# Optimization experiments

Measured on AMD Instinct MI355X. Metric: run time of the kernel, lower is better.

## Reference

```python
import jax, jax.numpy as jnp
import numpy as np

EMBED = 512
HEADS = 8
DIM_HEAD = 64          # embed_dim // 8
LANDMARKS = 256        # embed_dim // 2
PINV_ITERS = 6
RES_K = 33             # nystrom residual_conv_kernel default
SCALE = DIM_HEAD ** -0.5


def layer_norm(x, g, b, eps=1e-5):
    mu = x.mean(-1, keepdims=True)
    var = ((x - mu) ** 2).mean(-1, keepdims=True)
    return (x - mu) / jnp.sqrt(var + eps) * g + b


def moore_penrose_pinv(x, iters=PINV_ITERS):
    # iterative Moore-Penrose pseudo-inverse (lucidrains nystrom-attention)
    ax = jnp.abs(x)
    z = jnp.swapaxes(x, -1, -2) / (ax.sum(-1).max() * ax.sum(-2).max())
    I = jnp.eye(x.shape[-1], dtype=x.dtype)
    for _ in range(iters):
        xz = x @ z
        z = 0.25 * z @ (13. * I - xz @ (15. * I - xz @ (7. * I - xz)))
    return z


def nystrom_attention(x, w_qkv, w_out, b_out, res_k):
    b, n, _ = x.shape
    m = LANDMARKS
    pad = (m - n % m) % m
    xp = jnp.pad(x, ((0, 0), (pad, 0), (0, 0)))  # left-pad like F.pad(..., padding, 0)
    np_ = n + pad
    qkv = (xp @ w_qkv).reshape(b, np_, 3, HEADS, DIM_HEAD)
    q = qkv[:, :, 0].transpose(0, 2, 1, 3) * SCALE   # [b,h,np,dh]
    k = qkv[:, :, 1].transpose(0, 2, 1, 3)
    v = qkv[:, :, 2].transpose(0, 2, 1, 3)
    l = np_ // m
    q_l = q.reshape(b, HEADS, m, l, DIM_HEAD).mean(3)  # [b,h,m,dh]
    k_l = k.reshape(b, HEADS, m, l, DIM_HEAD).mean(3)
    attn1 = jax.nn.softmax(jnp.einsum('bhid,bhjd->bhij', q, k_l), -1)    # [b,h,np,m]
    attn2 = jax.nn.softmax(jnp.einsum('bhid,bhjd->bhij', q_l, k_l), -1)  # [b,h,m,m]
    attn3 = jax.nn.softmax(jnp.einsum('bhid,bhjd->bhij', q_l, k), -1)    # [b,h,m,np]
    out = (attn1 @ moore_penrose_pinv(attn2)) @ (attn3 @ v)              # [b,h,np,dh]
    # depthwise residual conv over the sequence dim, per head (shared across dh)
    v_c = v.transpose(0, 3, 1, 2).reshape(b * DIM_HEAD, HEADS, np_)
    res = jax.lax.conv_general_dilated(
        v_c, res_k[:, None, :], (1,), [(RES_K // 2, RES_K // 2)],
        dimension_numbers=('NCH', 'OIH', 'NCH'), feature_group_count=HEADS)
    out = out + res.reshape(b, DIM_HEAD, HEADS, np_).transpose(0, 2, 3, 1)
    out = out.transpose(0, 2, 1, 3).reshape(b, np_, HEADS * DIM_HEAD)
    out = out @ w_out + b_out
    return out[:, -n:]  # drop left padding


def dwconv2d(x, w, b, k):
    # x: [B,C,H,W], w: [C,1,k,k] depthwise
    y = jax.lax.conv_general_dilated(
        x, w, (1, 1), [(k // 2, k // 2)] * 2,
        dimension_numbers=('NCHW', 'OIHW', 'NCHW'), feature_group_count=x.shape[1])
    return y + b[None, :, None, None]


def ppeg(x, H, W, w7, b7, w5, b5, w3, b3):
    B, _, C = x.shape
    cls_tok, feat = x[:, :1], x[:, 1:]
    f = feat.transpose(0, 2, 1).reshape(B, C, H, W)
    y = f + dwconv2d(f, w7, b7, 7) + dwconv2d(f, w5, b5, 5) + dwconv2d(f, w3, b3, 3)
    y = y.reshape(B, C, H * W).transpose(0, 2, 1)
    return jnp.concatenate([cls_tok, y], axis=1)


def reference(h, w_fc1, b_fc1, cls_token,
              ln1_g, ln1_b, qkv1_w, out1_w, out1_b, res1_k,
              conv7_w, conv7_b, conv5_w, conv5_b, conv3_w, conv3_b,
              ln2_g, ln2_b, qkv2_w, out2_w, out2_b, res2_k,
              lnf_g, lnf_b):
    h = jax.nn.relu(h @ w_fc1 + b_fc1)                 # [B,N,512]
    B, N, C = h.shape
    _H = int(np.ceil(np.sqrt(N)))
    add = _H * _H - N
    h = jnp.concatenate([h, h[:, :add]], axis=1)       # square padding
    h = jnp.concatenate([jnp.broadcast_to(cls_token, (B, 1, C)), h], axis=1)
    h = h + nystrom_attention(layer_norm(h, ln1_g, ln1_b), qkv1_w, out1_w, out1_b, res1_k)
    h = ppeg(h, _H, _H, conv7_w, conv7_b, conv5_w, conv5_b, conv3_w, conv3_b)
    h = h + nystrom_attention(layer_norm(h, ln2_g, ln2_b), qkv2_w, out2_w, out2_b, res2_k)
    return layer_norm(h, lnf_g, lnf_b)[:, 0]           # [B,512]


def setup_inputs() -> dict:
    key = jax.random.key(0)
    ks = jax.random.split(key, 24)
    B, N, IN_DIM = 2, 4096, 1024
    w = lambda k, shape, s=0.02: jax.random.normal(k, shape, jnp.float32) * s
    z = lambda shape: jnp.zeros(shape, jnp.float32)
    o = lambda shape: jnp.ones(shape, jnp.float32)
    return {
        'h': jax.random.normal(ks[0], (B, N, IN_DIM), jnp.float32),
        'w_fc1': w(ks[1], (IN_DIM, EMBED)), 'b_fc1': z((EMBED,)),
        'cls_token': w(ks[2], (1, 1, EMBED)),
        'ln1_g': o((EMBED,)), 'ln1_b': z((EMBED,)),
        'qkv1_w': w(ks[3], (EMBED, 3 * HEADS * DIM_HEAD)),
        'out1_w': w(ks[4], (HEADS * DIM_HEAD, EMBED)), 'out1_b': z((EMBED,)),
        'res1_k': w(ks[5], (HEADS, RES_K), 0.1),
        'conv7_w': w(ks[6], (EMBED, 1, 7, 7), 0.05), 'conv7_b': z((EMBED,)),
        'conv5_w': w(ks[7], (EMBED, 1, 5, 5), 0.05), 'conv5_b': z((EMBED,)),
        'conv3_w': w(ks[8], (EMBED, 1, 3, 3), 0.05), 'conv3_b': z((EMBED,)),
        'ln2_g': o((EMBED,)), 'ln2_b': z((EMBED,)),
        'qkv2_w': w(ks[9], (EMBED, 3 * HEADS * DIM_HEAD)),
        'out2_w': w(ks[10], (HEADS * DIM_HEAD, EMBED)), 'out2_b': z((EMBED,)),
        'res2_k': w(ks[11], (HEADS, RES_K), 0.1),
        'lnf_g': o((EMBED,)), 'lnf_b': z((EMBED,)),
    }
```

## Files before the change

kernel.cpp:

```cpp
#include <hip/hip_runtime.h>
#include <hip/hip_bf16.h>

#define HEADS 8
#define DH 64
#define EMB 512
#define NP 4352
#define NTOK 4097
#define PADF 255
#define LM 256
#define SCALE 0.125f

typedef __attribute__((ext_vector_type(8))) short bf8;
typedef __attribute__((ext_vector_type(4))) float f4;
typedef __attribute__((ext_vector_type(8))) unsigned short us8;
typedef __attribute__((ext_vector_type(4))) unsigned short us4;
typedef unsigned short u16;

__device__ __forceinline__ u16 f2b(float f){
  union { float f; unsigned u; } x; x.f = f;
  unsigned r = x.u + 0x7fffu + ((x.u>>16)&1u);
  return (u16)(r>>16);
}
__device__ __forceinline__ float b2f(u16 h){
  union { unsigned u; float f; } x; x.u = ((unsigned)h)<<16;
  return x.f;
}

__device__ __forceinline__ void gload_lds(const u16* g, u16* l){
  __builtin_amdgcn_global_load_lds((const __attribute__((address_space(1))) void*)g,
                                   (__attribute__((address_space(3))) void*)l, 16, 0, 0);
}

template<int MODE>
__global__ __launch_bounds__(256)
void k_g128(const u16* __restrict__ A, const u16* __restrict__ B,
            float* __restrict__ C, u16* __restrict__ C16,
            int K, int lda, int ldb, int ldc,
            long sAb, long sAh, long sBb, long sBh, long sCb, long sCh, int nh,
            float alpha, const float* __restrict__ bias, int relu, int rowoff,
            int nx, int ksplit)
{
  int z = blockIdx.z;
  const u16* Ab = A + (long)(z/nh)*sAb + (long)(z%nh)*sAh;
  const u16* Bb = B + (long)(z/nh)*sBb + (long)(z%nh)*sBh;
  long cb = (long)(z/nh)*sCb + (long)(z%nh)*sCh;
  int bx = blockIdx.x % nx, kc = blockIdx.x / nx;
  int m0 = blockIdx.y*128, n0 = bx*128;
  int klen = K/ksplit, kbeg = kc*klen, nch = klen/32;
  __shared__ u16 As[2][4096];
  __shared__ u16 Bs[2][4096];
  int tid=threadIdx.x, w=tid>>6, lane=tid&63, q=lane>>4, lr=lane&15;
  int wrow=(w>>1)*64, wcol=(w&1)*64;
  int srow = tid>>2, scol = (tid&3)*8;
  const u16* ga  = Ab + (long)(m0+srow)*lda + kbeg + scol;
  const u16* ga2 = Ab + (long)(m0+64+srow)*lda + kbeg + scol;
  const u16* gb  = Bb + (long)(n0+srow)*ldb + kbeg + scol;
  const u16* gb2 = Bb + (long)(n0+64+srow)*ldb + kbeg + scol;
  int lo = srow*32 + scol;
  f4 acc[4][4] = {};
  auto stage = [&](int r, int c){
    gload_lds(ga  + c*32, &As[r][lo]);
    gload_lds(ga2 + c*32, &As[r][2048+lo]);
    gload_lds(gb  + c*32, &Bs[r][lo]);
    gload_lds(gb2 + c*32, &Bs[r][2048+lo]);
  };
  auto compute = [&](int r){
    bf8 af[4], bfr[4];
    #pragma unroll
    for(int rr=0;rr<4;rr++) af[rr]  = *(const bf8*)&As[r][(wrow + rr*16 + lr)*32 + q*8];
    #pragma unroll
    for(int t=0;t<4;t++) bfr[t] = *(const bf8*)&Bs[r][(wcol + t*16 + lr)*32 + q*8];
    #pragma unroll
    for(int rr=0;rr<4;rr++)
      #pragma unroll
      for(int t=0;t<4;t++)
        acc[rr][t] = __builtin_amdgcn_mfma_f32_16x16x32_bf16(af[rr], bfr[t], acc[rr][t], 0,0,0);
  };
  stage(0,0);
  __syncthreads();
  for(int c=1;c<nch;c++){
    stage(c&1, c);
    compute((c-1)&1);
    __syncthreads();
  }
  compute((nch-1)&1);
  #pragma unroll
  for(int r=0;r<4;r++){
    #pragma unroll
    for(int t=0;t<4;t++){
      #pragma unroll
      for(int e=0;e<4;e++){
        int gm = m0 + wrow + r*16 + q*4 + e;
        int gn = n0 + wcol + t*16 + lr;
        float v = acc[r][t][e]*alpha;
        if(MODE==4){
          if(bias && kc==0) v += bias[gn];
          if(gm>=rowoff) atomicAdd(&C[cb + (long)(gm-rowoff)*ldc + gn], v);
        } else {
          if(bias) v += bias[gn];
          if(relu) v = fmaxf(v,0.f);
          if(MODE==0) C[cb + (long)gm*ldc + gn] = v;
          else if(MODE==2) C16[cb + (long)gm*ldc + gn] = f2b(v);
          else { if(gm>=rowoff) C[cb + (long)(gm-rowoff)*ldc + gn] += v; }
        }
      }
    }
  }
}

template<int MODE>
__global__ __launch_bounds__(256)
void k_g64(const u16* __restrict__ A, const u16* __restrict__ B,
           float* __restrict__ C, u16* __restrict__ C16,
           int K, int lda, int ldb, int ldc,
           long sAb, long sAh, long sBb, long sBh, long sCb, long sCh, int nh,
           float alpha, const float* __restrict__ bias, int rowoff, int moff,
           int nx, int ksplit)
{
  int z = blockIdx.z;
  const u16* Ab = A + (long)(z/nh)*sAb + (long)(z%nh)*sAh;
  const u16* Bb = B + (long)(z/nh)*sBb + (long)(z%nh)*sBh;
  long cb = (long)(z/nh)*sCb + (long)(z%nh)*sCh;
  int bx = blockIdx.x % nx, kc = blockIdx.x / nx;
  int m0 = blockIdx.y*64 + moff, n0 = bx*64;
  int klen = K/ksplit, kbeg = kc*klen, nch = klen/32;
  __shared__ u16 As[2][2048];
  __shared__ u16 Bs[2][2048];
  int tid=threadIdx.x, w=tid>>6, lane=tid&63, q=lane>>4, lr=lane&15;
  int srow = tid>>2, scol = (tid&3)*8;
  const u16* ga = Ab + (long)(m0+srow)*lda + kbeg + scol;
  const u16* gb = Bb + (long)(n0+srow)*ldb + kbeg + scol;
  int lo = srow*32 + scol;
  f4 acc[4] = {};
  auto stage = [&](int r, int c){
    gload_lds(ga + c*32, &As[r][lo]);
    gload_lds(gb + c*32, &Bs[r][lo]);
  };
  auto compute = [&](int r){
    bf8 af = *(const bf8*)&As[r][(w*16 + lr)*32 + q*8];
    #pragma unroll
    for(int t=0;t<4;t++){
      bf8 bfr = *(const bf8*)&Bs[r][(t*16 + lr)*32 + q*8];
      acc[t] = __builtin_amdgcn_mfma_f32_16x16x32_bf16(af, bfr, acc[t], 0,0,0);
    }
  };
  stage(0,0);
  __syncthreads();
  for(int c=1;c<nch;c++){
    stage(c&1, c);
    compute((c-1)&1);
    __syncthreads();
  }
  compute((nch-1)&1);
  #pragma unroll
  for(int t=0;t<4;t++){
    #pragma unroll
    for(int e=0;e<4;e++){
      int gm = m0 + w*16 + q*4 + e;
      int gn = n0 + t*16 + lr;
      float v = acc[t][e]*alpha;
      if(MODE==0) C[cb + (long)gm*ldc + gn] = v;
      else if(MODE==2) C16[cb + (long)gm*ldc + gn] = f2b(v);
      else if(MODE==3) atomicAdd(&C[cb + (long)gm*ldc + gn], v);
      else if(MODE==5){
        v += bias[gn];
        if(gm>=rowoff) C[cb + (long)(gm-rowoff)*ldc + gn] += v;
      }
    }
  }
}

__global__ __launch_bounds__(256)
void k_pg3(const u16* __restrict__ Ah, const u16* __restrict__ Al,
           const u16* __restrict__ Bh, const u16* __restrict__ Bl,
           u16* __restrict__ Oh, u16* __restrict__ Ol, float na, float nd,
           u16* __restrict__ TOh, u16* __restrict__ TOl, float ta, float td)
{
  long zo = (long)blockIdx.z*65536;
  int m0 = blockIdx.y*32, n0 = blockIdx.x*64;
  __shared__ u16 S[2][6144];
  int tid=threadIdx.x, w=tid>>6, lane=tid&63, q=lane>>4, lr=lane&15;
  int t2 = tid & 127;
  const u16* srcA = (tid<128 ? Ah : Al) + zo + (long)(m0 + (t2>>2))*256 + (t2&3)*8;
  const u16* srcBh = Bh + zo + (long)(n0 + (tid>>2))*256 + (tid&3)*8;
  const u16* srcBl = Bl + zo + (long)(n0 + (tid>>2))*256 + (tid&3)*8;
  f4 acc[2] = {};
  auto stage = [&](int r, int c){
    gload_lds(srcA  + c*32, &S[r][tid*8]);
    gload_lds(srcBh + c*32, &S[r][2048 + tid*8]);
    gload_lds(srcBl + c*32, &S[r][4096 + tid*8]);
  };
  int mrow = (w>>1)*16 + lr;
  auto compute = [&](int r){
    bf8 ah = *(const bf8*)&S[r][mrow*32 + q*8];
    bf8 al = *(const bf8*)&S[r][1024 + mrow*32 + q*8];
    #pragma unroll
    for(int t=0;t<2;t++){
      int nrow = (w&1)*32 + t*16 + lr;
      bf8 bh = *(const bf8*)&S[r][2048 + nrow*32 + q*8];
      bf8 bl = *(const bf8*)&S[r][4096 + nrow*32 + q*8];
      acc[t] = __builtin_amdgcn_mfma_f32_16x16x32_bf16(ah, bh, acc[t], 0,0,0);
      acc[t] = __builtin_amdgcn_mfma_f32_16x16x32_bf16(ah, bl, acc[t], 0,0,0);
      acc[t] = __builtin_amdgcn_mfma_f32_16x16x32_bf16(al, bh, acc[t], 0,0,0);
    }
  };
  stage(0,0);
  __syncthreads();
  #pragma unroll
  for(int c=1;c<8;c++){
    stage(c&1, c);
    compute((c-1)&1);
    __syncthreads();
  }
  compute(1);
  #pragma unroll
  for(int t=0;t<2;t++){
    int gn = n0 + (w&1)*32 + t*16 + lr;
    if(Oh){
      #pragma unroll
      for(int r=0;r<4;r++){
        int gm = m0 + (w>>1)*16 + q*4 + r;
        float v = na*acc[t][r] + ((gm==gn)?nd:0.f);
        u16 h = f2b(v);
        long o = zo + (long)gm*256 + gn;
        Oh[o] = h; Ol[o] = f2b(v - b2f(h));
      }
    }
    if(TOh){
      us4 th, tl;
      #pragma unroll
      for(int r=0;r<4;r++){
        int gm = m0 + (w>>1)*16 + q*4 + r;
        float v = ta*acc[t][r] + ((gm==gn)?td:0.f);
        u16 h = f2b(v);
        th[r] = h; tl[r] = f2b(v - b2f(h));
      }
      long o = zo + (long)gn*256 + (m0 + (w>>1)*16 + q*4);
      *(us4*)&TOh[o] = th; *(us4*)&TOl[o] = tl;
    }
  }
}

__global__ __launch_bounds__(256)
void k_att3(const u16* __restrict__ qkv16, const u16* __restrict__ ql,
            const u16* __restrict__ vT, float* __restrict__ partO,
            float* __restrict__ pm, float* __restrict__ pl)
{
  int kc = blockIdx.x, jt = blockIdx.y, z = blockIdx.z;
  int b = z>>3, h = z&7;
  __shared__ u16 SQ[64*64];
  __shared__ u16 SK[2][64*64];
  __shared__ u16 SV[2][64*64];
  __shared__ u16 SP[64*64];
  int tid=threadIdx.x, w=tid>>6, lane=tid&63, q=lane>>4, lr=lane&15;
  const u16* kb = qkv16 + (long)b*NP*1536 + 512 + h*64;
  const u16* vb = vT + (long)z*64*NP;
  int t00 = kc*256;
  {
    const u16* qb = ql + (long)z*16384 + jt*64*64;
    #pragma unroll
    for(int p=0;p<2;p++){
      int idx = tid + p*256; int row = idx>>3; int js = ((idx&7)^(row&7))<<3;
      gload_lds(qb + row*64 + js, &SQ[idx*8]);
    }
  }
  auto stageKV = [&](int r, int i){
    int t0 = t00 + i*64;
    #pragma unroll
    for(int p=0;p<2;p++){
      int idx = tid + p*256; int row = idx>>3; int js = ((idx&7)^(row&7))<<3;
      gload_lds(kb + (long)(t0+row)*1536 + js, &SK[r][idx*8]);
      gload_lds(vb + (long)row*NP + t0 + js, &SV[r][idx*8]);
    }
  };
  stageKV(0,0);
  __syncthreads();
  int ar = w*16+lr;
  bf8 af0 = *(const bf8*)&SQ[ar*64 + ((q^(ar&7))<<3)];
  bf8 af1 = *(const bf8*)&SQ[ar*64 + (((q|4)^(ar&7))<<3)];
  f4 o[4] = {};
  float m[4] = {-3e38f,-3e38f,-3e38f,-3e38f};
  float l[4] = {0.f,0.f,0.f,0.f};
  for(int i=0;i<4;i++){
    int cur = i&1;
    if(i<3) stageKV(cur^1, i+1);
    f4 s[4] = {};
    #pragma unroll
    for(int t=0;t<4;t++){
      int br = t*16+lr;
      bf8 b0 = *(const bf8*)&SK[cur][br*64 + ((q^(br&7))<<3)];
      bf8 b1 = *(const bf8*)&SK[cur][br*64 + (((q|4)^(br&7))<<3)];
      s[t] = __builtin_amdgcn_mfma_f32_16x16x32_bf16(af0, b0, s[t], 0,0,0);
      s[t] = __builtin_amdgcn_mfma_f32_16x16x32_bf16(af1, b1, s[t], 0,0,0);
    }
    float tm[4];
    #pragma unroll
    for(int e=0;e<4;e++) tm[e] = fmaxf(fmaxf(s[0][e],s[1][e]), fmaxf(s[2][e],s[3][e]));
    #pragma unroll
    for(int sh=1; sh<16; sh<<=1)
      #pragma unroll
      for(int e=0;e<4;e++) tm[e] = fmaxf(tm[e], __shfl_xor(tm[e], sh));
    float rs[4];
    #pragma unroll
    for(int e=0;e<4;e++){
      float mn = fmaxf(m[e], tm[e]);
      float sc = expf(m[e]-mn);
      m[e] = mn;
      l[e] *= sc;
      rs[e] = 0.f;
      o[0][e]*=sc; o[1][e]*=sc; o[2][e]*=sc; o[3][e]*=sc;
    }
    #pragma unroll
    for(int t=0;t<4;t++)
      #pragma unroll
      for(int e=0;e<4;e++){
        float p = expf(s[t][e]-m[e]);
        rs[e] += p;
        int prow = w*16+q*4+e, pcol = t*16+lr;
        SP[prow*64 + (((pcol>>3)^(prow&7))<<3) + (pcol&7)] = f2b(p);
      }
    #pragma unroll
    for(int sh=1; sh<16; sh<<=1)
      #pragma unroll
      for(int e=0;e<4;e++) rs[e] += __shfl_xor(rs[e], sh);
    #pragma unroll
    for(int e=0;e<4;e++) l[e] += rs[e];
    int pr = w*16+lr;
    #pragma unroll
    for(int ks=0;ks<2;ks++){
      bf8 pa = *(const bf8*)&SP[pr*64 + (((ks*4+q)^(pr&7))<<3)];
      #pragma unroll
      for(int t2=0;t2<4;t2++){
        int rr = t2*16+lr;
        bf8 vv = *(const bf8*)&SV[cur][rr*64 + (((ks*4+q)^(rr&7))<<3)];
        o[t2] = __builtin_amdgcn_mfma_f32_16x16x32_bf16(pa, vv, o[t2], 0,0,0);
      }
    }
    __syncthreads();
  }
  long pb = (long)(z*17+kc)*256 + jt*64 + w*16;
  #pragma unroll
  for(int e=0;e<4;e++){
    int jg = q*4+e;
    #pragma unroll
    for(int t2=0;t2<4;t2++)
      partO[(pb + jg)*64 + t2*16 + lr] = o[t2][e];
    if(lr==0){ pm[pb + jg] = m[e]; pl[pb + jg] = l[e]; }
  }
}

__global__ __launch_bounds__(128)
void k_mrg3(const float* __restrict__ partO, const float* __restrict__ pm,
            const float* __restrict__ pl, u16* __restrict__ avbT16)
{
  int jq = blockIdx.x, z = blockIdx.y, tid = threadIdx.x;
  int j0 = jq*16;
  __shared__ float wk[16][17];
  __shared__ u16 T[16][72];
  if(tid < 16){
    int j = j0 + tid;
    float mm[17];
    float M = -3e38f;
    #pragma unroll
    for(int kc=0;kc<17;kc++){ mm[kc]=pm[(z*17+kc)*256 + j]; M=fmaxf(M,mm[kc]); }
    float s = 0.f;
    #pragma unroll
    for(int kc=0;kc<17;kc++){ float e=expf(mm[kc]-M); wk[tid][kc]=e; s+=e*pl[(z*17+kc)*256 + j]; }
    float inv = 1.f/s;
    #pragma unroll
    for(int kc=0;kc<17;kc++) wk[tid][kc]*=inv;
  }
  __syncthreads();
  float acc[8];
  #pragma unroll
  for(int p=0;p<8;p++) acc[p]=0.f;
  for(int kc=0;kc<17;kc++){
    long base = ((long)(z*17+kc)*256 + j0)*64;
    #pragma unroll
    for(int p=0;p<8;p++){
      int idx = tid + p*128;
      acc[p] += wk[idx>>6][kc]*partO[base + idx];
    }
  }
  #pragma unroll
  for(int p=0;p<8;p++){ int idx = tid + p*128; T[idx>>6][idx&63] = f2b(acc[p]); }
  __syncthreads();
  int d = tid>>1, jh = (tid&1)*8;
  us8 vv;
  #pragma unroll
  for(int u=0;u<8;u++) vv[u] = T[jh+u][d];
  *(us8*)&avbT16[(long)(z*64+d)*256 + j0 + jh] = vv;
}

__global__ __launch_bounds__(256)
void k_att1(const u16* __restrict__ qkv16, const u16* __restrict__ kl,
            const u16* __restrict__ zavT, float* __restrict__ Qc)
{
  int z = blockIdx.y, b = z>>3, h = z&7;
  int m0 = blockIdx.x*64;
  __shared__ u16 SQ[64*64];
  __shared__ u16 SKL[256*64];
  __shared__ u16 SZV[64*256];
  int tid=threadIdx.x, w=tid>>6, lane=tid&63, q=lane>>4, lr=lane&15;
  {
    const u16* qb = qkv16 + (long)b*NP*1536 + h*64;
    #pragma unroll
    for(int p=0;p<2;p++){
      int idx = tid + p*256; int row = idx>>3, c8 = (idx&7)*8;
      gload_lds(qb + (long)(m0+row)*1536 + c8, &SQ[row*64 + c8]);
    }
    const u16* kb = kl + (long)z*16384;
    #pragma unroll
    for(int p=0;p<8;p++){
      int idx = tid + p*256; int row = idx>>3, c8 = (idx&7)*8;
      gload_lds(kb + row*64 + c8, &SKL[row*64 + c8]);
    }
    const u16* zb = zavT + (long)z*16384;
    #pragma unroll
    for(int p=0;p<8;p++){
      int idx = tid + p*256; int row = idx>>5, c8 = (idx&31)*8;
      gload_lds(zb + row*256 + c8, &SZV[row*256 + c8]);
    }
  }
  __syncthreads();
  f4 acc[16] = {};
  {
    bf8 af0 = *(const bf8*)&SQ[(w*16+lr)*64 + q*8];
    bf8 af1 = *(const bf8*)&SQ[(w*16+lr)*64 + 32 + q*8];
    #pragma unroll
    for(int t=0;t<16;t++){
      bf8 b0 = *(const bf8*)&SKL[(t*16+lr)*64 + q*8];
      bf8 b1 = *(const bf8*)&SKL[(t*16+lr)*64 + 32 + q*8];
      acc[t] = __builtin_amdgcn_mfma_f32_16x16x32_bf16(af0, b0, acc[t], 0,0,0);
      acc[t] = __builtin_amdgcn_mfma_f32_16x16x32_bf16(af1, b1, acc[t], 0,0,0);
    }
  }
  float mx[4] = {-1e30f,-1e30f,-1e30f,-1e30f};
  #pragma unroll
  for(int t=0;t<16;t++)
    #pragma unroll
    for(int e=0;e<4;e++) mx[e] = fmaxf(mx[e], acc[t][e]*SCALE);
  #pragma unroll
  for(int s=1;s<16;s<<=1)
    #pragma unroll
    for(int e=0;e<4;e++) mx[e] = fmaxf(mx[e], __shfl_xor(mx[e], s));
  float sm[4] = {0.f,0.f,0.f,0.f};
  #pragma unroll
  for(int t=0;t<16;t++)
    #pragma unroll
    for(int e=0;e<4;e++){ float p = expf(acc[t][e]*SCALE - mx[e]); acc[t][e]=p; sm[e]+=p; }
  #pragma unroll
  for(int s=1;s<16;s<<=1)
    #pragma unroll
    for(int e=0;e<4;e++) sm[e] += __shfl_xor(sm[e], s);
  float inv[4];
  #pragma unroll
  for(int e=0;e<4;e++) inv[e] = 1.f/sm[e];
  __syncthreads();
  u16* PS = SKL;
  #pragma unroll
  for(int t=0;t<16;t++)
    #pragma unroll
    for(int e=0;e<4;e++)
      PS[(w*16 + q*4 + e)*256 + t*16 + lr] = f2b(acc[t][e]*inv[e]);
  __syncthreads();
  f4 acc2[4] = {};
  #pragma unroll
  for(int ks=0;ks<8;ks++){
    bf8 af = *(const bf8*)&PS[(w*16+lr)*256 + ks*32 + q*8];
    #pragma unroll
    for(int t=0;t<4;t++){
      bf8 bf_ = *(const bf8*)&SZV[(t*16+lr)*256 + ks*32 + q*8];
      acc2[t] = __builtin_amdgcn_mfma_f32_16x16x32_bf16(af, bf_, acc2[t], 0,0,0);
    }
  }
  #pragma unroll
  for(int t=0;t<4;t++)
    #pragma unroll
    for(int r=0;r<4;r++){
      int gm = m0 + w*16 + q*4 + r;
      int gd = t*16 + lr;
      Qc[((long)b*NP + gm)*512 + h*64 + gd] = acc2[t][r];
    }
}

__global__ __launch_bounds__(256)
void k_smw32(float* __restrict__ X){
  long row = (long)blockIdx.x*4 + (threadIdx.x>>6);
  int lane = threadIdx.x & 63;
  float* p = X + row*256;
  float4 v = *(float4*)&p[lane*4];
  float m = fmaxf(fmaxf(v.x,v.y),fmaxf(v.z,v.w));
  for(int s=32;s;s>>=1) m = fmaxf(m, __shfl_xor(m, s));
  float e0=expf(v.x-m), e1=expf(v.y-m), e2=expf(v.z-m), e3=expf(v.w-m);
  float sum = e0+e1+e2+e3;
  for(int s=32;s;s>>=1) sum += __shfl_xor(sum, s);
  float inv = 1.f/sum;
  float4 o = {e0*inv, e1*inv, e2*inv, e3*inv};
  *(float4*)&p[lane*4] = o;
}

__global__ void k_wT(const float* __restrict__ in, u16* __restrict__ out, int K, int N){
  int n0=blockIdx.x*32, k0=blockIdx.y*32, tid=threadIdx.x;
  __shared__ float T[32][33];
  int lr=tid&31, lc=tid>>5;
  #pragma unroll
  for(int p=0;p<4;p++) T[lc+8*p][lr] = in[(long)(k0+lc+8*p)*N + n0+lr];
  __syncthreads();
  #pragma unroll
  for(int p=0;p<4;p++) out[(long)(n0+lc+8*p)*K + k0+lr] = f2b(T[lr][lc+8*p]);
}

__global__ __launch_bounds__(256)
void k_vT(const u16* __restrict__ qkv16, u16* __restrict__ vT){
  int t0=blockIdx.x*64, h=blockIdx.y, b=blockIdx.z, tid=threadIdx.x;
  __shared__ u16 T[64][72];
  const u16* src = qkv16 + (long)b*NP*1536 + 1024 + h*64;
  for(int s=0;s<2;s++){
    int idx=tid+s*256; int row=idx>>3, c8=(idx&7)*8;
    *(us8*)&T[row][c8] = *(const us8*)&src[(long)(t0+row)*1536 + c8];
  }
  __syncthreads();
  u16* dst = vT + ((long)(b*8+h)*64)*NP;
  int d = tid>>2, j0=(tid&3)*16;
  us8 v0,v1;
  #pragma unroll
  for(int jj=0;jj<8;jj++){ v0[jj]=T[j0+jj][d]; v1[jj]=T[j0+8+jj][d]; }
  *(us8*)&dst[(long)d*NP + t0 + j0]     = v0;
  *(us8*)&dst[(long)d*NP + t0 + j0 + 8] = v1;
}

__global__ void k_cvt16(const float* __restrict__ in, u16* __restrict__ out, long n){
  long i = (long)blockIdx.x*256 + threadIdx.x;
  if(i<n) out[i] = f2b(in[i]);
}

__global__ void k_cls(const float* __restrict__ cls, float* __restrict__ seq){
  int b = blockIdx.x;
  seq[(long)b*NTOK*EMB + threadIdx.x] = cls[threadIdx.x];
}

__global__ void k_ln_pad(const float* __restrict__ seq, u16* __restrict__ xp,
                         const float* __restrict__ g, const float* __restrict__ bb){
  int b = blockIdx.y, i = blockIdx.x, tid = threadIdx.x;
  u16* out = xp + ((long)b*NP + i)*EMB;
  if(i < PADF){ out[tid]=0; out[tid+256]=0; return; }
  const float* x = seq + ((long)b*NTOK + (i-PADF))*EMB;
  float v0 = x[tid], v1 = x[tid+256];
  __shared__ float red[256];
  red[tid]=v0+v1; __syncthreads();
  for(int s=128;s>0;s>>=1){ if(tid<s) red[tid]+=red[tid+s]; __syncthreads(); }
  float mu = red[0]*(1.0f/512.0f); __syncthreads();
  float d0=v0-mu, d1=v1-mu;
  red[tid]=d0*d0+d1*d1; __syncthreads();
  for(int s=128;s>0;s>>=1){ if(tid<s) red[tid]+=red[tid+s]; __syncthreads(); }
  float rstd = rsqrtf(red[0]*(1.0f/512.0f) + 1e-5f);
  out[tid]     = f2b(d0*rstd*g[tid]     + bb[tid]);
  out[tid+256] = f2b(d1*rstd*g[tid+256] + bb[tid+256]);
}

__global__ void k_landmarks(const u16* __restrict__ qkv, u16* __restrict__ q_l, u16* __restrict__ k_l){
  int j = blockIdx.x, h = blockIdx.y, b = blockIdx.z, d = threadIdx.x;
  const u16* base = qkv + (long)b*NP*1536 + h*64 + d;
  float sq=0.f, sk=0.f;
  for(int l=0;l<17;l++){
    long row = (long)(j*17+l)*1536;
    sq += b2f(base[row]);
    sk += b2f(base[row+512]);
  }
  long o = (((long)b*HEADS + h)*LM + j)*DH + d;
  q_l[o] = f2b(sq * (SCALE/17.0f));
  k_l[o] = f2b(sk * (1.0f/17.0f));
}

__global__ void k_pinv_norm(const float* __restrict__ A2, float* __restrict__ rmax, float* __restrict__ cmax){
  int z = blockIdx.x, tid = threadIdx.x;
  const float* X = A2 + (long)z*65536;
  float rs=0.f, cs=0.f;
  for(int j=0;j<256;j++){ rs += fabsf(X[tid*256+j]); cs += fabsf(X[j*256+tid]); }
  __shared__ float r1[256], r2[256];
  r1[tid]=rs; r2[tid]=cs; __syncthreads();
  for(int s=128;s>0;s>>=1){ if(tid<s){ r1[tid]=fmaxf(r1[tid],r1[tid+s]); r2[tid]=fmaxf(r2[tid],r2[tid+s]); } __syncthreads(); }
  if(tid==0){ rmax[z]=r1[0]; cmax[z]=r2[0]; }
}

__global__ void k_pair_init(const float* __restrict__ att2,
    const float* __restrict__ rmax, const float* __restrict__ cmax,
    u16* __restrict__ Xh, u16* __restrict__ Xl,
    u16* __restrict__ Zh, u16* __restrict__ Zl,
    u16* __restrict__ Zth, u16* __restrict__ Ztl)
{
  long zo = (long)blockIdx.z*65536;
  int i0 = blockIdx.y*64, j0 = blockIdx.x*64;
  float rm=0.f, cm=0.f;
  for(int t=0;t<16;t++){ rm=fmaxf(rm,rmax[t]); cm=fmaxf(cm,cmax[t]); }
  float inv = 1.0f/(rm*cm);
  __shared__ float T[64][68];
  int tid = threadIdx.x;
  int li = tid>>2, jc = (tid&3)*16;
  #pragma unroll
  for(int u=0;u<4;u++){
    float4 v = *(const float4*)&att2[zo + (long)(i0+li)*256 + j0 + jc + u*4];
    T[li][jc+u*4]=v.x; T[li][jc+u*4+1]=v.y; T[li][jc+u*4+2]=v.z; T[li][jc+u*4+3]=v.w;
    long o = zo + (long)(i0+li)*256 + j0 + jc + u*4;
    float vv[4] = {v.x,v.y,v.z,v.w};
    us4 xh, xl, zth, ztl;
    #pragma unroll
    for(int c=0;c<4;c++){
      u16 h = f2b(vv[c]); xh[c]=h; xl[c]=f2b(vv[c]-b2f(h));
      float zt = vv[c]*inv;
      u16 h2 = f2b(zt); zth[c]=h2; ztl[c]=f2b(zt-b2f(h2));
    }
    *(us4*)&Xh[o]=xh; *(us4*)&Xl[o]=xl; *(us4*)&Zth[o]=zth; *(us4*)&Ztl[o]=ztl;
  }
  __syncthreads();
  int lj = tid>>2, ic = (tid&3)*16;
  #pragma unroll
  for(int r=0;r<16;r++){
    float x = T[ic+r][lj]*inv;
    u16 h = f2b(x);
    long o = zo + (long)(j0+lj)*256 + i0 + ic + r;
    Zh[o]=h; Zl[o]=f2b(x-b2f(h));
  }
}

__global__ __launch_bounds__(256)
void k_rconv(const u16* __restrict__ qkv16, const float* __restrict__ resk,
             const float* __restrict__ Qin, u16* __restrict__ Qo16){
  int t0 = blockIdx.x*64, h = blockIdx.y, b = blockIdx.z;
  __shared__ float V[96*64];
  const u16* vb = qkv16 + (long)b*NP*1536 + 1024 + h*64;
  int tid = threadIdx.x;
  #pragma unroll
  for(int s=0;s<3;s++){
    int idx = tid + s*256;
    int row = idx>>3, c8 = (idx&7)*8;
    int p = t0 - 16 + row;
    if(p>=0 && p<NP){
      us8 v = *(const us8*)&vb[(long)p*1536 + c8];
      #pragma unroll
      for(int jj=0;jj<8;jj++) V[row*64+c8+jj] = b2f(v[jj]);
    } else {
      #pragma unroll
      for(int jj=0;jj<8;jj++) V[row*64+c8+jj] = 0.f;
    }
  }
  __syncthreads();
  int d = tid&63, lt = (tid>>6)*16;
  float acc[16] = {};
  #pragma unroll
  for(int s=0;s<48;s++){
    float val = V[(lt+s)*64 + d];
    #pragma unroll
    for(int j=0;j<16;j++){
      int tap = s - j;
      if(tap>=0 && tap<33) acc[j] += resk[h*33+tap]*val;
    }
  }
  #pragma unroll
  for(int j=0;j<16;j++){
    long idx = ((long)b*NP + t0 + lt + j)*EMB + h*64 + d;
    Qo16[idx] = f2b(Qin[idx] + acc[j]);
  }
}

__global__ __launch_bounds__(256)
void k_ppeg(const float* __restrict__ seq, float* __restrict__ out,
    const float* __restrict__ w7,const float* __restrict__ b7,
    const float* __restrict__ w5,const float* __restrict__ b5,
    const float* __restrict__ w3,const float* __restrict__ b3){
  int b = blockIdx.z, cg = blockIdx.y;
  int rp = blockIdx.x>>1, xs = blockIdx.x&1;
  int ch0 = cg*64;
  __shared__ float s7[64*49], s5[64*25], s3[64*9], sbias[64];
  int tid = threadIdx.x;
  for(int i=tid;i<64*49;i+=256) s7[i] = w7[ch0*49+i];
  for(int i=tid;i<64*25;i+=256) s5[i] = w5[ch0*25+i];
  for(int i=tid;i<64*9;i+=256)  s3[i] = w3[ch0*9+i];
  if(tid<64) sbias[tid] = b7[ch0+tid]+b5[ch0+tid]+b3[ch0+tid];
  if(cg==0 && blockIdx.x==0){
    out[(long)b*NTOK*EMB + tid]       = seq[(long)b*NTOK*EMB + tid];
    out[(long)b*NTOK*EMB + 256 + tid] = seq[(long)b*NTOK*EMB + 256 + tid];
  }
  __syncthreads();
  int c = tid & 63;
  int y = rp*4 + (tid>>6);
  const float* sbase = seq + (long)b*NTOK*EMB + EMB + (ch0 + c);
  float* obase = out + (long)b*NTOK*EMB + EMB + (ch0 + c);
  const float* W7 = &s7[c*49];
  const float* W5 = &s5[c*25];
  const float* W3 = &s3[c*9];
  float bsum = sbias[c];
  for(int xc=0;xc<4;xc++){
    int xb = xs*32 + xc*8;
    float acc[8];
    #pragma unroll
    for(int j=0;j<8;j++) acc[j] = sbase[(long)(y*64+xb+j)*EMB] + bsum;
    #pragma unroll
    for(int dy=-3;dy<=3;dy++){
      int yy = y+dy;
      if(yy<0||yy>=64) continue;
      float v[14];
      #pragma unroll
      for(int u=0;u<14;u++){
        int xx = xb + u - 3;
        v[u] = (xx>=0 && xx<64) ? sbase[(long)(yy*64+xx)*EMB] : 0.f;
      }
      #pragma unroll
      for(int dx=-3;dx<=3;dx++){
        float wsum = W7[(dy+3)*7+(dx+3)];
        if(dy>=-2&&dy<=2&&dx>=-2&&dx<=2) wsum += W5[(dy+2)*5+(dx+2)];
        if(dy>=-1&&dy<=1&&dx>=-1&&dx<=1) wsum += W3[(dy+1)*3+(dx+1)];
        #pragma unroll
        for(int j=0;j<8;j++) acc[j] += v[j+dx+3]*wsum;
      }
    }
    #pragma unroll
    for(int j=0;j<8;j++) obase[(long)(y*64+xb+j)*EMB] = acc[j];
  }
}

__global__ void k_final_ln(const float* __restrict__ seq, const float* __restrict__ g,
                           const float* __restrict__ bb, float* __restrict__ out){
  int b = blockIdx.x, tid = threadIdx.x;
  const float* x = seq + (long)b*NTOK*EMB;
  float v0 = x[tid], v1 = x[tid+256];
  __shared__ float red[256];
  red[tid]=v0+v1; __syncthreads();
  for(int s=128;s>0;s>>=1){ if(tid<s) red[tid]+=red[tid+s]; __syncthreads(); }
  float mu = red[0]*(1.0f/512.0f); __syncthreads();
  float d0=v0-mu, d1=v1-mu;
  red[tid]=d0*d0+d1*d1; __syncthreads();
  for(int s=128;s>0;s>>=1){ if(tid<s) red[tid]+=red[tid+s]; __syncthreads(); }
  float rstd = rsqrtf(red[0]*(1.0f/512.0f) + 1e-5f);
  out[b*512+tid]     = d0*rstd*g[tid]     + bb[tid];
  out[b*512+tid+256] = d1*rstd*g[tid+256] + bb[tid+256];
}

extern "C" void kernel_launch(void* const* d_in, const int* in_sizes, int n_in,
                              void* d_out, int out_size, void* d_ws, size_t ws_size,
                              hipStream_t stream) {
  const float* in[24];
  for(int i=0;i<24;i++) in[i] = (const float*)d_in[i];

  float* W = (float*)d_ws;
  size_t off = 0;
  float* seqA = W+off; off += 4195328;
  float* seqB = W+off; off += 4195328;
  float* att2 = W+off; off += 1048576;
  float* Qc   = W+off; off += 4456448;
  float* partO= W+off; off += 17825792;
  float* pm   = W+off; off += 69632;
  float* pl   = W+off; off += 69632;
  u16* xpb    = (u16*)(W+off); off += 2228224;
  u16* qkvb16 = (u16*)(W+off); off += 6684672;
  u16* vT16   = (u16*)(W+off); off += 2228224;
  u16* q_l16  = (u16*)(W+off); off += 131072;
  u16* k_l16  = (u16*)(W+off); off += 131072;
  u16* avbT16 = (u16*)(W+off); off += 131072;
  u16* zavT16 = (u16*)(W+off); off += 131072;
  u16* Qc16   = (u16*)(W+off); off += 2228224;
  u16* qkvwT1 = (u16*)(W+off); off += 393216;
  u16* qkvwT2 = (u16*)(W+off); off += 393216;
  u16* outwT1 = (u16*)(W+off); off += 131072;
  u16* outwT2 = (u16*)(W+off); off += 131072;
  u16* pairs  = (u16*)(W+off); off += 9437184;
  float* rmax = W+off; off += 16;
  float* cmax = W+off; off += 16;
  if (ws_size < off*sizeof(float)) return;

  u16* h16   = pairs;
  u16* wfc1T = pairs + 8388608;

  const long PB = 1048576;
  u16 *Xh=pairs, *Xl=pairs+PB;
  u16 *Z0h=pairs+2*PB, *Z0l=pairs+3*PB, *Z0th=pairs+4*PB, *Z0tl=pairs+5*PB;
  u16 *Z1h=pairs+6*PB, *Z1l=pairs+7*PB, *Z1th=pairs+8*PB, *Z1tl=pairs+9*PB;
  u16 *Ph=pairs+10*PB, *Pl=pairs+11*PB;
  u16 *Tth=pairs+12*PB, *Ttl=pairs+13*PB;
  u16 *Uth=pairs+14*PB, *Utl=pairs+15*PB;
  u16 *Vth=pairs+16*PB, *Vtl=pairs+17*PB;

  k_cvt16<<<32768,256,0,stream>>>(in[0], h16, 8388608L);
  k_wT<<<dim3(16,32),256,0,stream>>>(in[1],  wfc1T, 1024, 512);
  k_wT<<<dim3(48,16),256,0,stream>>>(in[6],  qkvwT1, 512, 1536);
  k_wT<<<dim3(48,16),256,0,stream>>>(in[18], qkvwT2, 512, 1536);
  k_wT<<<dim3(16,16),256,0,stream>>>(in[7],  outwT1, 512, 512);
  k_wT<<<dim3(16,16),256,0,stream>>>(in[19], outwT2, 512, 512);

  k_g128<0><<<dim3(4,32,2),256,0,stream>>>(h16, wfc1T, seqA+EMB, nullptr,
      1024, 1024,1024,512, 4194304L,0, 0,0, (long)NTOK*EMB,0, 1, 1.0f, in[2], 1, 0, 4, 1);
  k_cls<<<2,512,0,stream>>>(in[3], seqA);

  auto attention = [&](float* seq, const float* lng,const float* lnb,
                       const u16* qkvwT, const u16* outwT, const float* outb, const float* resk){
    k_ln_pad<<<dim3(NP,2),256,0,stream>>>(seq, xpb, lng, lnb);
    k_g128<2><<<dim3(12,34,2),256,0,stream>>>(xpb, qkvwT, nullptr, qkvb16,
        512, 512,512,1536, (long)NP*512,0, 0,0, (long)NP*1536,0, 1, 1.0f, nullptr, 0, 0, 12, 1);
    k_landmarks<<<dim3(LM,HEADS,2),64,0,stream>>>(qkvb16, q_l16, k_l16);
    k_vT<<<dim3(68,8,2),256,0,stream>>>(qkvb16, vT16);
    k_g128<0><<<dim3(2,2,16),256,0,stream>>>(q_l16, k_l16, att2, nullptr,
        64, 64,64,256, 0,16384, 0,16384, 0,65536, 16, 1.0f, nullptr, 0, 0, 2, 1);
    k_smw32<<<1024,256,0,stream>>>(att2);
    k_pinv_norm<<<16,256,0,stream>>>(att2, rmax, cmax);
    k_pair_init<<<dim3(4,4,16),256,0,stream>>>(att2, rmax, cmax, Xh,Xl, Z0h,Z0l, Z0th,Z0tl);
    dim3 pgrid(4,8,16);
    for(int it=0; it<6; it++){
      u16 *Zh_=(it&1)?Z1h:Z0h, *Zl_=(it&1)?Z1l:Z0l, *Zth_=(it&1)?Z1th:Z0th, *Ztl_=(it&1)?Z1tl:Z0tl;
      u16 *Nh_=(it&1)?Z0h:Z1h, *Nl_=(it&1)?Z0l:Z1l, *Nth_=(it&1)?Z0th:Z1th, *Ntl_=(it&1)?Z0tl:Z1tl;
      k_pg3<<<pgrid,256,0,stream>>>(Xh,Xl, Zth_,Ztl_, Ph,Pl,1.0f,0.f, Tth,Ttl,-1.0f,7.f);
      k_pg3<<<pgrid,256,0,stream>>>(Ph,Pl, Tth,Ttl, nullptr,nullptr,0.f,0.f, Uth,Utl,-1.0f,15.f);
      k_pg3<<<pgrid,256,0,stream>>>(Ph,Pl, Uth,Utl, nullptr,nullptr,0.f,0.f, Vth,Vtl,-1.0f,13.f);
      if(it<5) k_pg3<<<pgrid,256,0,stream>>>(Zh_,Zl_, Vth,Vtl, Nh_,Nl_,0.25f,0.f, Nth_,Ntl_,0.25f,0.f);
      else     k_pg3<<<pgrid,256,0,stream>>>(Zh_,Zl_, Vth,Vtl, Nh_,Nl_,0.25f,0.f, nullptr,nullptr,0.f,0.f);
    }
    k_att3<<<dim3(17,4,16),256,0,stream>>>(qkvb16, q_l16, vT16, partO, pm, pl);
    k_mrg3<<<dim3(16,16),128,0,stream>>>(partO, pm, pl, avbT16);
    k_g64<2><<<dim3(4,1,16),256,0,stream>>>(avbT16, Z0h, nullptr, zavT16,
        256, 256,256,256, 0,16384L, 0,65536L, 0,16384L, 16, 1.0f, nullptr, 0, 0, 4, 1);
    k_att1<<<dim3(68,16),256,0,stream>>>(qkvb16, k_l16, zavT16, Qc);
    k_rconv<<<dim3(68,8,2),256,0,stream>>>(qkvb16, resk, Qc, Qc16);
    k_g64<5><<<dim3(8,65,2),256,0,stream>>>(Qc16, outwT, seq, nullptr,
        512, 512,512,512, (long)NP*512,0, 0,0, (long)NTOK*EMB,0, 1, 1.0f, outb, PADF, 192, 8, 1);
  };

  attention(seqA, in[4], in[5], qkvwT1, outwT1, in[8], in[9]);
  k_ppeg<<<dim3(32,8,2),256,0,stream>>>(seqA, seqB, in[10],in[11],in[12],in[13],in[14],in[15]);
  attention(seqB, in[16], in[17], qkvwT2, outwT2, in[20], in[21]);
  k_final_ln<<<2,256,0,stream>>>(seqB, in[22], in[23], (float*)d_out);
}
```

Before: 986.9 us.

## Restructure pinv iteration to compute next XZ as P·V, swizzle att1 LDS, batch landmarks

The Newton-Schulz pinv loop now uses the identity X·Z_next = 0.25·(X·Z)·V, so one fused kernel (k_pg3b) produces both Z_next = 0.25·Z·V and P_next = 0.25·P·V along with the 7I−P transpose. This removes one dependent GEMM launch per iteration and drops the transposed-Z buffers. Separately, k_att1 applies an XOR swizzle to its LDS tiles to avoid bank conflicts, and k_landmarks packs four landmarks per 256-thread block. The algebraic rewrite may change rounding, since P is no longer recomputed from X each iteration.

Result: faster. 917.5 us (-7.0%).

```diff
diff --git a/kernel.cpp b/kernel.cpp
--- a/kernel.cpp
+++ b/kernel.cpp
@@ -242,6 +242,85 @@
 }
 
 __global__ __launch_bounds__(256)
+void k_pg3b(const u16* __restrict__ Zh, const u16* __restrict__ Zl,
+            const u16* __restrict__ Ph, const u16* __restrict__ Pl,
+            const u16* __restrict__ Bh, const u16* __restrict__ Bl,
+            u16* __restrict__ Ozh, u16* __restrict__ Ozl,
+            u16* __restrict__ Oyh, u16* __restrict__ Oyl,
+            u16* __restrict__ Tyh, u16* __restrict__ Tyl)
+{
+  long zo = (long)blockIdx.z*65536;
+  int ysel = blockIdx.y>>3;
+  int m0 = (blockIdx.y&7)*32, n0 = blockIdx.x*64;
+  const u16* Ah = ysel ? Ph : Zh;
+  const u16* Al = ysel ? Pl : Zl;
+  __shared__ u16 S[2][6144];
+  int tid=threadIdx.x, w=tid>>6, lane=tid&63, q=lane>>4, lr=lane&15;
+  int t2 = tid & 127;
+  const u16* srcA = (tid<128 ? Ah : Al) + zo + (long)(m0 + (t2>>2))*256 + (t2&3)*8;
+  const u16* srcBh = Bh + zo + (long)(n0 + (tid>>2))*256 + (tid&3)*8;
+  const u16* srcBl = Bl + zo + (long)(n0 + (tid>>2))*256 + (tid&3)*8;
+  f4 acc[2] = {};
+  auto stage = [&](int r, int c){
+    gload_lds(srcA  + c*32, &S[r][tid*8]);
+    gload_lds(srcBh + c*32, &S[r][2048 + tid*8]);
+    gload_lds(srcBl + c*32, &S[r][4096 + tid*8]);
+  };
+  int mrow = (w>>1)*16 + lr;
+  auto compute = [&](int r){
+    bf8 ah = *(const bf8*)&S[r][mrow*32 + q*8];
+    bf8 al = *(const bf8*)&S[r][1024 + mrow*32 + q*8];
+    #pragma unroll
+    for(int t=0;t<2;t++){
+      int nrow = (w&1)*32 + t*16 + lr;
+      bf8 bh = *(const bf8*)&S[r][2048 + nrow*32 + q*8];
+      bf8 bl = *(const bf8*)&S[r][4096 + nrow*32 + q*8];
+      acc[t] = __builtin_amdgcn_mfma_f32_16x16x32_bf16(ah, bh, acc[t], 0,0,0);
+      acc[t] = __builtin_amdgcn_mfma_f32_16x16x32_bf16(ah, bl, acc[t], 0,0,0);
+      acc[t] = __builtin_amdgcn_mfma_f32_16x16x32_bf16(al, bh, acc[t], 0,0,0);
+    }
+  };
+  stage(0,0);
+  __syncthreads();
+  #pragma unroll
+  for(int c=1;c<8;c++){
+    stage(c&1, c);
+    compute((c-1)&1);
+    __syncthreads();
+  }
+  compute(1);
+  #pragma unroll
+  for(int t=0;t<2;t++){
+    int gn = n0 + (w&1)*32 + t*16 + lr;
+    if(!ysel){
+      #pragma unroll
+      for(int r=0;r<4;r++){
+        int gm = m0 + (w>>1)*16 + q*4 + r;
+        float v = 0.25f*acc[t][r];
+        u16 h = f2b(v);
+        long o = zo + (long)gm*256 + gn;
+        Ozh[o] = h; Ozl[o] = f2b(v - b2f(h));
+      }
+    } else {
+      us4 th, tl;
+      #pragma unroll
+      for(int r=0;r<4;r++){
+        int gm = m0 + (w>>1)*16 + q*4 + r;
+        float v = 0.25f*acc[t][r];
+        u16 h = f2b(v);
+        long o = zo + (long)gm*256 + gn;
+        Oyh[o] = h; Oyl[o] = f2b(v - b2f(h));
+        float tv = -v + ((gm==gn)?7.f:0.f);
+        u16 h2 = f2b(tv);
+        th[r] = h2; tl[r] = f2b(tv - b2f(h2));
+      }
+      long o = zo + (long)gn*256 + (m0 + (w>>1)*16 + q*4);
+      *(us4*)&Tyh[o] = th; *(us4*)&Tyl[o] = tl;
+    }
+  }
+}
+
+__global__ __launch_bounds__(256)
 void k_att3(const u16* __restrict__ qkv16, const u16* __restrict__ ql,
             const u16* __restrict__ vT, float* __restrict__ partO,
             float* __restrict__ pm, float* __restrict__ pl)
@@ -406,31 +485,33 @@
     const u16* qb = qkv16 + (long)b*NP*1536 + h*64;
     #pragma unroll
     for(int p=0;p<2;p++){
-      int idx = tid + p*256; int row = idx>>3, c8 = (idx&7)*8;
-      gload_lds(qb + (long)(m0+row)*1536 + c8, &SQ[row*64 + c8]);
+      int idx = tid + p*256; int row = idx>>3; int js = ((idx&7)^(row&7))<<3;
+      gload_lds(qb + (long)(m0+row)*1536 + js, &SQ[idx*8]);
     }
     const u16* kb = kl + (long)z*16384;
     #pragma unroll
     for(int p=0;p<8;p++){
-      int idx = tid + p*256; int row = idx>>3, c8 = (idx&7)*8;
-      gload_lds(kb + row*64 + c8, &SKL[row*64 + c8]);
+      int idx = tid + p*256; int row = idx>>3; int js = ((idx&7)^(row&7))<<3;
+      gload_lds(kb + row*64 + js, &SKL[idx*8]);
     }
     const u16* zb = zavT + (long)z*16384;
     #pragma unroll
     for(int p=0;p<8;p++){
-      int idx = tid + p*256; int row = idx>>5, c8 = (idx&31)*8;
-      gload_lds(zb + row*256 + c8, &SZV[row*256 + c8]);
+      int idx = tid + p*256; int row = idx>>5; int cs = ((idx&31)^(row&7))<<3;
+      gload_lds(zb + row*256 + cs, &SZV[idx*8]);
     }
   }
   __syncthreads();
   f4 acc[16] = {};
   {
-    bf8 af0 = *(const bf8*)&SQ[(w*16+lr)*64 + q*8];
-    bf8 af1 = *(const bf8*)&SQ[(w*16+lr)*64 + 32 + q*8];
+    int ar = w*16+lr;
+    bf8 af0 = *(const bf8*)&SQ[ar*64 + ((q^(ar&7))<<3)];
+    bf8 af1 = *(const bf8*)&SQ[ar*64 + (((q|4)^(ar&7))<<3)];
     #pragma unroll
     for(int t=0;t<16;t++){
-      bf8 b0 = *(const bf8*)&SKL[(t*16+lr)*64 + q*8];
-      bf8 b1 = *(const bf8*)&SKL[(t*16+lr)*64 + 32 + q*8];
+      int br = t*16+lr;
+      bf8 b0 = *(const bf8*)&SKL[br*64 + ((q^(br&7))<<3)];
+      bf8 b1 = *(const bf8*)&SKL[br*64 + (((q|4)^(br&7))<<3)];
       acc[t] = __builtin_amdgcn_mfma_f32_16x16x32_bf16(af0, b0, acc[t], 0,0,0);
       acc[t] = __builtin_amdgcn_mfma_f32_16x16x32_bf16(af1, b1, acc[t], 0,0,0);
     }
@@ -461,16 +542,20 @@
   #pragma unroll
   for(int t=0;t<16;t++)
     #pragma unroll
-    for(int e=0;e<4;e++)
-      PS[(w*16 + q*4 + e)*256 + t*16 + lr] = f2b(acc[t][e]*inv[e]);
+    for(int e=0;e<4;e++){
+      int prow = w*16 + q*4 + e, pcol = t*16 + lr;
+      PS[prow*256 + (((pcol>>3)^(prow&7))<<3) + (pcol&7)] = f2b(acc[t][e]*inv[e]);
+    }
   __syncthreads();
   f4 acc2[4] = {};
+  int pr = w*16+lr;
   #pragma unroll
   for(int ks=0;ks<8;ks++){
-    bf8 af = *(const bf8*)&PS[(w*16+lr)*256 + ks*32 + q*8];
+    bf8 af = *(const bf8*)&PS[pr*256 + (((ks*4+q)^(pr&7))<<3)];
     #pragma unroll
     for(int t=0;t<4;t++){
-      bf8 bf_ = *(const bf8*)&SZV[(t*16+lr)*256 + ks*32 + q*8];
+      int rr = t*16+lr;
+      bf8 bf_ = *(const bf8*)&SZV[rr*256 + (((ks*4+q)^(rr&7))<<3)];
       acc2[t] = __builtin_amdgcn_mfma_f32_16x16x32_bf16(af, bf_, acc2[t], 0,0,0);
     }
   }
@@ -560,7 +645,7 @@
 }
 
 __global__ void k_landmarks(const u16* __restrict__ qkv, u16* __restrict__ q_l, u16* __restrict__ k_l){
-  int j = blockIdx.x, h = blockIdx.y, b = blockIdx.z, d = threadIdx.x;
+  int j = blockIdx.x*4 + (threadIdx.x>>6), h = blockIdx.y, b = blockIdx.z, d = threadIdx.x&63;
   const u16* base = qkv + (long)b*NP*1536 + h*64 + d;
   float sq=0.f, sk=0.f;
   for(int l=0;l<17;l++){
@@ -773,10 +858,12 @@
   u16* wfc1T = pairs + 8388608;
 
   const long PB = 1048576;
-  u16 *Xh=pairs, *Xl=pairs+PB;
-  u16 *Z0h=pairs+2*PB, *Z0l=pairs+3*PB, *Z0th=pairs+4*PB, *Z0tl=pairs+5*PB;
-  u16 *Z1h=pairs+6*PB, *Z1l=pairs+7*PB, *Z1th=pairs+8*PB, *Z1tl=pairs+9*PB;
-  u16 *Ph=pairs+10*PB, *Pl=pairs+11*PB;
+  u16 *Xh=pairs,        *Xl=pairs+PB;
+  u16 *Z0h=pairs+2*PB,  *Z0l=pairs+3*PB;
+  u16 *Z0th=pairs+4*PB, *Z0tl=pairs+5*PB;
+  u16 *Z1h=pairs+6*PB,  *Z1l=pairs+7*PB;
+  u16 *P0h=pairs+8*PB,  *P0l=pairs+9*PB;
+  u16 *P1h=pairs+10*PB, *P1l=pairs+11*PB;
   u16 *Tth=pairs+12*PB, *Ttl=pairs+13*PB;
   u16 *Uth=pairs+14*PB, *Utl=pairs+15*PB;
   u16 *Vth=pairs+16*PB, *Vtl=pairs+17*PB;
@@ -797,7 +884,7 @@
     k_ln_pad<<<dim3(NP,2),256,0,stream>>>(seq, xpb, lng, lnb);
     k_g128<2><<<dim3(12,34,2),256,0,stream>>>(xpb, qkvwT, nullptr, qkvb16,
         512, 512,512,1536, (long)NP*512,0, 0,0, (long)NP*1536,0, 1, 1.0f, nullptr, 0, 0, 12, 1);
-    k_landmarks<<<dim3(LM,HEADS,2),64,0,stream>>>(qkvb16, q_l16, k_l16);
+    k_landmarks<<<dim3(64,HEADS,2),256,0,stream>>>(qkvb16, q_l16, k_l16);
     k_vT<<<dim3(68,8,2),256,0,stream>>>(qkvb16, vT16);
     k_g128<0><<<dim3(2,2,16),256,0,stream>>>(q_l16, k_l16, att2, nullptr,
         64, 64,64,256, 0,16384, 0,16384, 0,65536, 16, 1.0f, nullptr, 0, 0, 2, 1);
@@ -805,14 +892,18 @@
     k_pinv_norm<<<16,256,0,stream>>>(att2, rmax, cmax);
     k_pair_init<<<dim3(4,4,16),256,0,stream>>>(att2, rmax, cmax, Xh,Xl, Z0h,Z0l, Z0th,Z0tl);
     dim3 pgrid(4,8,16);
+    k_pg3<<<pgrid,256,0,stream>>>(Xh,Xl, Z0th,Z0tl, P0h,P0l,1.0f,0.f, Tth,Ttl,-1.0f,7.f);
     for(int it=0; it<6; it++){
-      u16 *Zh_=(it&1)?Z1h:Z0h, *Zl_=(it&1)?Z1l:Z0l, *Zth_=(it&1)?Z1th:Z0th, *Ztl_=(it&1)?Z1tl:Z0tl;
-      u16 *Nh_=(it&1)?Z0h:Z1h, *Nl_=(it&1)?Z0l:Z1l, *Nth_=(it&1)?Z0th:Z1th, *Ntl_=(it&1)?Z0tl:Z1tl;
-      k_pg3<<<pgrid,256,0,stream>>>(Xh,Xl, Zth_,Ztl_, Ph,Pl,1.0f,0.f, Tth,Ttl,-1.0f,7.f);
-      k_pg3<<<pgrid,256,0,stream>>>(Ph,Pl, Tth,Ttl, nullptr,nullptr,0.f,0.f, Uth,Utl,-1.0f,15.f);
-      k_pg3<<<pgrid,256,0,stream>>>(Ph,Pl, Uth,Utl, nullptr,nullptr,0.f,0.f, Vth,Vtl,-1.0f,13.f);
-      if(it<5) k_pg3<<<pgrid,256,0,stream>>>(Zh_,Zl_, Vth,Vtl, Nh_,Nl_,0.25f,0.f, Nth_,Ntl_,0.25f,0.f);
-      else     k_pg3<<<pgrid,256,0,stream>>>(Zh_,Zl_, Vth,Vtl, Nh_,Nl_,0.25f,0.f, nullptr,nullptr,0.f,0.f);
+      u16 *Zh_=(it&1)?Z1h:Z0h, *Zl_=(it&1)?Z1l:Z0l;
+      u16 *Nh_=(it&1)?Z0h:Z1h, *Nl_=(it&1)?Z0l:Z1l;
+      u16 *Pch=(it&1)?P1h:P0h, *Pcl=(it&1)?P1l:P0l;
+      u16 *Pnh=(it&1)?P0h:P1h, *Pnl=(it&1)?P0l:P1l;
+      k_pg3<<<pgrid,256,0,stream>>>(Pch,Pcl, Tth,Ttl, nullptr,nullptr,0.f,0.f, Uth,Utl,-1.0f,15.f);
+      k_pg3<<<pgrid,256,0,stream>>>(Pch,Pcl, Uth,Utl, nullptr,nullptr,0.f,0.f, Vth,Vtl,-1.0f,13.f);
+      if(it<5) k_pg3b<<<dim3(4,16,16),256,0,stream>>>(Zh_,Zl_, Pch,Pcl, Vth,Vtl,
+                                                      Nh_,Nl_, Pnh,Pnl, Tth,Ttl);
+      else     k_pg3<<<pgrid,256,0,stream>>>(Zh_,Zl_, Vth,Vtl, Nh_,Nl_,0.25f,0.f,
+                                             nullptr,nullptr,0.f,0.f);
     }
     k_att3<<<dim3(17,4,16),256,0,stream>>>(qkvb16, q_l16, vT16, partO, pm, pl);
     k_mrg3<<<dim3(16,16),128,0,stream>>>(partO, pm, pl, avbT16);
```
